# Kernel optimization log

Measured on AMD Instinct MI355X. Metric: run time of the kernel, lower is better.

Reference implementation:

```python
import jax, jax.numpy as jnp
import numpy as np

BN_EPS = 1e-5

def binarize_ste(x):
    # sign() in forward; identity (straight-through) in backward, matching the
    # weight.data / input.data hack in BinarizeConv2d.
    return x + jax.lax.stop_gradient(jnp.sign(x) - x)


def setup_inputs() -> dict:
    key = jax.random.key(0)
    k1, k2, k3, k4 = jax.random.split(key, 4)
    N, Cin, H, W = 16, 32, 224, 224
    Cout, K = 32, 3
    x = jax.random.normal(k1, (N, Cin, H, W), dtype=jnp.float32)
    weight = jax.random.normal(k2, (Cout, Cin, K, K), dtype=jnp.float32) * 0.1
    gamma = jax.random.uniform(k3, (Cout,), dtype=jnp.float32, minval=0.5, maxval=1.5)
    beta = jax.random.normal(k4, (Cout,), dtype=jnp.float32) * 0.1
    return {"x": x, "weight": weight, "gamma": gamma, "beta": beta}


def reference(x, weight, gamma, beta):
    # BinarizeConv2d: binarize input iff C != 3, always binarize weights.
    xb = binarize_ste(x) if x.shape[1] != 3 else x
    wb = binarize_ste(weight)
    y = jax.lax.conv_general_dilated(
        xb, wb,
        window_strides=(1, 1),
        padding=((1, 1), (1, 1)),
        dimension_numbers=("NCHW", "OIHW", "NCHW"),
    )  # [N, Cout, H, W]
    # BatchNorm2d in training mode: per-channel batch statistics over (N, H, W).
    mean = jnp.mean(y, axis=(0, 2, 3))
    var = jnp.var(y, axis=(0, 2, 3))
    inv = jax.lax.rsqrt(var + BN_EPS)
    yn = (y - mean[None, :, None, None]) * inv[None, :, None, None]
    return yn * gamma[None, :, None, None] + beta[None, :, None, None]
```

## Files before the change

### kernel.cpp

```cpp
#include <hip/hip_runtime.h>
#include <stdint.h>

#define NB 16
#define CC 32
#define HH 224
#define WWID 224
#define HWS (HH*WWID)
#define NHWT (NB*HWS)
#define STRIPS (NHWT/4)
#define SPI (HWS/4)
#define SPR (WWID/4)
#define PBLK (STRIPS/256)

#define PITCH 232
#define PROWS 226
#define IMGW (PITCH*PROWS)

typedef float    f4 __attribute__((ext_vector_type(4)));
typedef unsigned u4 __attribute__((ext_vector_type(4)));
typedef unsigned u2 __attribute__((ext_vector_type(2)));

#define WS_WSIGN 0
#define WS_WNZ   2048
#define WS_BASE  4096
#define WS_FLAGW 5248
#define WS_SSUM  5376
#define WS_SSQ   5632
#define WS_BLKF  6144
#define WS_XS    12288
#define WS_XNZ   (12288 + (size_t)NB*IMGW*4)

__global__ void __launch_bounds__(256) pack_x4(
        const float* __restrict__ x, const float* __restrict__ w,
        unsigned* __restrict__ xs, unsigned* __restrict__ xnz,
        unsigned* __restrict__ wsg, unsigned* __restrict__ wnz,
        int* __restrict__ flagw, unsigned* __restrict__ blkflag,
        int* __restrict__ baset, int* __restrict__ s_sum,
        unsigned long long* __restrict__ s_sq) {
    __shared__ unsigned s_sg[288];
    __shared__ int allnz;
    __shared__ unsigned s_zf[4];

    if (blockIdx.x == 0) {
        if (threadIdx.x == 0) allnz = 1;
        if (threadIdx.x < CC) { s_sum[threadIdx.x] = 0; s_sq[threadIdx.x] = 0ull; }
        __syncthreads();
        for (int k = threadIdx.x; k < 288; k += 256) {
            int co = k / 9, tap = k % 9;
            unsigned bits = 0, nz = 0;
            for (int ci = 0; ci < CC; ++ci) {
                float v = w[(co * CC + ci) * 9 + tap];
                bits |= (v > 0.f ? 1u : 0u) << ci;
                nz   |= (v != 0.f ? 1u : 0u) << ci;
            }
            wsg[k] = bits; wnz[k] = nz; s_sg[k] = bits;
            if (nz != 0xffffffffu) atomicAnd(&allnz, 0);
        }
        __syncthreads();
        if (threadIdx.x == 0) *flagw = allnz;
        for (int k = threadIdx.x; k < 288; k += 256) {
            int cls = k >> 5, co = k & 31;
            int hc = cls / 3, wc = cls % 3;
            int nv = 0, corr = 0;
            #pragma unroll
            for (int kh = 0; kh < 3; ++kh)
                #pragma unroll
                for (int kw = 0; kw < 3; ++kw) {
                    bool inv = (hc == 0 && kh == 0) || (hc == 2 && kh == 2) ||
                               (wc == 0 && kw == 0) || (wc == 2 && kw == 2);
                    if (inv) corr += __popc(s_sg[co * 9 + kh * 3 + kw]);
                    else     nv++;
                }
            baset[k] = 32 * nv + 2 * corr;
        }
    }

    int t = blockIdx.x * 256 + threadIdx.x;
    int n = t / SPI, rem = t - n * SPI;
    int h = rem / SPR, w0 = (rem - h * SPR) * 4;
    const float* base = x + (size_t)n * CC * HWS + h * WWID + w0;
    unsigned b0=0,b1=0,b2=0,b3=0, z0=0,z1=0,z2=0,z3=0;
    #pragma unroll
    for (int c = 0; c < CC; ++c) {
        f4 v = __builtin_nontemporal_load((const f4*)(base + (size_t)c * HWS));
        b0 |= (v.x > 0.f ? (1u<<c) : 0u);  z0 |= (v.x != 0.f ? (1u<<c) : 0u);
        b1 |= (v.y > 0.f ? (1u<<c) : 0u);  z1 |= (v.y != 0.f ? (1u<<c) : 0u);
        b2 |= (v.z > 0.f ? (1u<<c) : 0u);  z2 |= (v.z != 0.f ? (1u<<c) : 0u);
        b3 |= (v.w > 0.f ? (1u<<c) : 0u);  z3 |= (v.w != 0.f ? (1u<<c) : 0u);
    }
    size_t rowb = (size_t)n * IMGW + (h + 1) * PITCH;
    size_t d = rowb + 1 + w0;
    xs[d+0]=b0; xs[d+1]=b1; xs[d+2]=b2; xs[d+3]=b3;
    xnz[d+0]=z0; xnz[d+1]=z1; xnz[d+2]=z2; xnz[d+3]=z3;

    if (w0 == 0)        { xs[rowb] = 0;       xnz[rowb] = 0; }
    if (w0 == WWID - 4) { xs[rowb + 225] = 0; xnz[rowb + 225] = 0; }
    if (h == 0) {
        size_t tr = (size_t)n * IMGW;
        #pragma unroll
        for (int j = 0; j < 4; ++j) { xs[tr + 1 + w0 + j] = 0; xnz[tr + 1 + w0 + j] = 0; }
        if (w0 == 0)        { xs[tr] = 0;       xnz[tr] = 0; }
        if (w0 == WWID - 4) { xs[tr + 225] = 0; xnz[tr + 225] = 0; }
    }
    if (h == HH - 1) {
        size_t br = (size_t)n * IMGW + (size_t)(PROWS - 1) * PITCH;
        #pragma unroll
        for (int j = 0; j < 4; ++j) { xs[br + 1 + w0 + j] = 0; xnz[br + 1 + w0 + j] = 0; }
        if (w0 == 0)        { xs[br] = 0;       xnz[br] = 0; }
        if (w0 == WWID - 4) { xs[br + 225] = 0; xnz[br + 225] = 0; }
    }

    bool hasz = (z0 & z1 & z2 & z3) != 0xffffffffu;
    bool anyz = __any(hasz);
    int wid = threadIdx.x >> 6, lane = threadIdx.x & 63;
    if (lane == 0) s_zf[wid] = anyz ? 1u : 0u;
    __syncthreads();
    if (threadIdx.x == 0)
        blkflag[blockIdx.x] = s_zf[0] | s_zf[1] | s_zf[2] | s_zf[3];
}

__device__ __forceinline__ void loadwin(const unsigned* __restrict__ p, unsigned a[6]) {
    u4 lo = *(const u4*)p;
    u2 hi = *(const u2*)(p + 4);
    a[0]=lo.x; a[1]=lo.y; a[2]=lo.z; a[3]=lo.w; a[4]=hi.x; a[5]=hi.y;
}

__device__ __forceinline__ void ad4(const unsigned a0[6], const unsigned a1[6],
                                    const unsigned a2[6],
                                    const unsigned* __restrict__ q, int ad[4]) {
    unsigned q0=q[0],q1=q[1],q2=q[2],q3=q[3],q4=q[4],q5=q[5],q6=q[6],q7=q[7],q8=q[8];
    #pragma unroll
    for (int px = 0; px < 4; ++px) {
        ad[px] = __popc(a0[px]^q0) + __popc(a0[px+1]^q1) + __popc(a0[px+2]^q2)
               + __popc(a1[px]^q3) + __popc(a1[px+1]^q4) + __popc(a1[px+2]^q5)
               + __popc(a2[px]^q6) + __popc(a2[px+1]^q7) + __popc(a2[px+2]^q8);
    }
}

__device__ __forceinline__ void y4_slowc(const unsigned a0[6], const unsigned a1[6],
                                         const unsigned a2[6], const unsigned z0[6],
                                         const unsigned z1[6], const unsigned z2[6],
                                         const unsigned* __restrict__ qs,
                                         const unsigned* __restrict__ qz, int y[4]) {
    #pragma unroll
    for (int px = 0; px < 4; ++px) {
        int am = 0, ad = 0;
        #pragma unroll
        for (int kw = 0; kw < 3; ++kw) {
            unsigned m0 = z0[px+kw] & qz[kw];
            unsigned m1 = z1[px+kw] & qz[3+kw];
            unsigned m2 = z2[px+kw] & qz[6+kw];
            am += __popc(m0) + __popc(m1) + __popc(m2);
            ad += __popc((a0[px+kw]^qs[kw])   & m0)
                + __popc((a1[px+kw]^qs[3+kw]) & m1)
                + __popc((a2[px+kw]^qs[6+kw]) & m2);
        }
        y[px] = am - 2 * ad;
    }
}

__device__ __forceinline__ unsigned zf_load(const unsigned* __restrict__ blkflag, int t) {
    unsigned zv = blkflag[t] | blkflag[t + 256] | blkflag[t + 512];
    if (t < PBLK - 768) zv |= blkflag[t + 768];
    return zv;
}

__device__ __forceinline__ void deswizzle(int B, int* cobase, int* sblk) {
    int xcd = B & 7;
    int r = B >> 3;
    *cobase = (r & 3) * 8;
    *sblk = xcd + 8 * (r >> 2);
}

__global__ void __launch_bounds__(256, 8) convstats(
        const unsigned* __restrict__ xs, const unsigned* __restrict__ xnz,
        const unsigned* __restrict__ wsg, const unsigned* __restrict__ wnz,
        const int* __restrict__ baset, const int* __restrict__ flagw,
        const unsigned* __restrict__ blkflag, int* __restrict__ s_sum,
        unsigned long long* __restrict__ s_sq) {
    __shared__ int sb[288];
    __shared__ unsigned s_zf[4];
    __shared__ int red[4][8][17];

    int cobase, sblk;
    deswizzle(blockIdx.x, &cobase, &sblk);
    int sid = sblk * 256 + threadIdx.x;
    int n = sid / SPI, rem = sid - n * SPI;
    int h = rem / SPR, w0 = (rem - h * SPR) * 4;
    size_t off = (size_t)n * IMGW + h * PITCH + w0;

    unsigned a0[6], a1[6], a2[6];
    loadwin(xs + off, a0); loadwin(xs + off + PITCH, a1); loadwin(xs + off + 2*PITCH, a2);

    int t = threadIdx.x, wid = t >> 6, lane = t & 63;
    unsigned zv = zf_load(blkflag, t);
    int fw = *flagw;
    for (int i = t; i < 288; i += 256) sb[i] = baset[i];
    bool anyz = __any(zv != 0);
    if (lane == 0) s_zf[wid] = anyz ? 1u : 0u;
    __syncthreads();
    bool fast = (fw != 0) && ((s_zf[0] | s_zf[1] | s_zf[2] | s_zf[3]) == 0u);

    int sacc[8], qacc[8];
    if (fast) {
        int hc = (h == 0) ? 0 : ((h == HH-1) ? 6 : 3);
        int c0 = (hc + ((w0 == 0) ? 0 : 1)) * 32;
        int c1 = (hc + 1) * 32;
        int c3 = (hc + ((w0 == WWID-4) ? 2 : 1)) * 32;
        #pragma unroll
        for (int u = 0; u < 8; ++u) {
            int co = cobase + u;
            int ad[4];
            ad4(a0, a1, a2, wsg + co * 9, ad);
            int y0 = sb[c0 + co] - 2 * ad[0];
            int y1 = sb[c1 + co] - 2 * ad[1];
            int y2 = sb[c1 + co] - 2 * ad[2];
            int y3 = sb[c3 + co] - 2 * ad[3];
            sacc[u] = y0 + y1 + y2 + y3;
            qacc[u] = y0*y0 + y1*y1 + y2*y2 + y3*y3;
        }
    } else {
        unsigned z0[6], z1[6], z2[6];
        loadwin(xnz + off, z0); loadwin(xnz + off + PITCH, z1); loadwin(xnz + off + 2*PITCH, z2);
        #pragma unroll
        for (int u = 0; u < 8; ++u) {
            int co = cobase + u;
            int y[4];
            y4_slowc(a0, a1, a2, z0, z1, z2, wsg + co * 9, wnz + co * 9, y);
            sacc[u] = y[0]+y[1]+y[2]+y[3];
            qacc[u] = y[0]*y[0]+y[1]*y[1]+y[2]*y[2]+y[3]*y[3];
        }
    }

    #pragma unroll
    for (int o2 = 32; o2 >= 8; o2 >>= 1) {
        #pragma unroll
        for (int u = 0; u < 8; ++u) {
            sacc[u] += __shfl_down(sacc[u], o2);
            qacc[u] += __shfl_down(qacc[u], o2);
        }
    }
    if (lane < 8) {
        #pragma unroll
        for (int u = 0; u < 8; ++u) {
            red[wid][lane][u]     = sacc[u];
            red[wid][lane][8 + u] = qacc[u];
        }
    }
    __syncthreads();
    if (t < 128) {
        int u16 = t >> 3, s = t & 7;
        int v = red[0][s][u16] + red[1][s][u16] + red[2][s][u16] + red[3][s][u16];
        v += __shfl_down(v, 4); v += __shfl_down(v, 2); v += __shfl_down(v, 1);
        if (s == 0) {
            if (u16 < 8) atomicAdd(&s_sum[cobase + u16], v);
            else         atomicAdd(&s_sq[cobase + u16 - 8],
                                   (unsigned long long)(long long)v);
        }
    }
}

__global__ void __launch_bounds__(256, 8) convnorm(
        const unsigned* __restrict__ xs, const unsigned* __restrict__ xnz,
        const unsigned* __restrict__ wsg, const unsigned* __restrict__ wnz,
        const int* __restrict__ baset, const int* __restrict__ flagw,
        const unsigned* __restrict__ blkflag, const int* __restrict__ s_sum,
        const unsigned long long* __restrict__ s_sq,
        const float* __restrict__ gamma, const float* __restrict__ beta,
        float* __restrict__ out) {
    __shared__ int sb[288];
    __shared__ float s_sc[32], s_sh[32];
    __shared__ unsigned s_zf[4];

    int cobase, sblk;
    deswizzle(blockIdx.x, &cobase, &sblk);
    int sid = sblk * 256 + threadIdx.x;
    int n = sid / SPI, rem = sid - n * SPI;
    int h = rem / SPR, w0 = (rem - h * SPR) * 4;
    size_t off = (size_t)n * IMGW + h * PITCH + w0;

    unsigned a0[6], a1[6], a2[6];
    loadwin(xs + off, a0); loadwin(xs + off + PITCH, a1); loadwin(xs + off + 2*PITCH, a2);

    int t = threadIdx.x, wid = t >> 6, lane = t & 63;
    unsigned zv = zf_load(blkflag, t);
    int fw = *flagw;
    for (int i = t; i < 288; i += 256) sb[i] = baset[i];
    if (t < 32) {
        int c = t;
        double mean = (double)s_sum[c] / (double)NHWT;
        double var  = (double)(long long)s_sq[c] / (double)NHWT - mean * mean;
        float inv = (float)(1.0 / sqrt(var + 1e-5));
        float g = gamma[c] * inv;
        s_sc[c] = g;
        s_sh[c] = beta[c] - (float)mean * g;
    }
    bool anyz = __any(zv != 0);
    if (lane == 0) s_zf[wid] = anyz ? 1u : 0u;
    __syncthreads();
    bool fast = (fw != 0) && ((s_zf[0] | s_zf[1] | s_zf[2] | s_zf[3]) == 0u);

    float* on = out + (size_t)(n * CC + cobase) * HWS + h * WWID + w0;
    if (fast) {
        int hc = (h == 0) ? 0 : ((h == HH-1) ? 6 : 3);
        int c0 = (hc + ((w0 == 0) ? 0 : 1)) * 32;
        int c1 = (hc + 1) * 32;
        int c3 = (hc + ((w0 == WWID-4) ? 2 : 1)) * 32;
        #pragma unroll
        for (int u = 0; u < 8; ++u) {
            int co = cobase + u;
            int ad[4];
            ad4(a0, a1, a2, wsg + co * 9, ad);
            int y0 = sb[c0 + co] - 2 * ad[0];
            int y1 = sb[c1 + co] - 2 * ad[1];
            int y2 = sb[c1 + co] - 2 * ad[2];
            int y3 = sb[c3 + co] - 2 * ad[3];
            float sc = s_sc[co], sh = s_sh[co];
            f4 o = { fmaf((float)y0, sc, sh), fmaf((float)y1, sc, sh),
                     fmaf((float)y2, sc, sh), fmaf((float)y3, sc, sh) };
            *(f4*)(on + (size_t)u * HWS) = o;
        }
    } else {
        unsigned z0[6], z1[6], z2[6];
        loadwin(xnz + off, z0); loadwin(xnz + off + PITCH, z1); loadwin(xnz + off + 2*PITCH, z2);
        #pragma unroll
        for (int u = 0; u < 8; ++u) {
            int co = cobase + u;
            int y[4];
            y4_slowc(a0, a1, a2, z0, z1, z2, wsg + co * 9, wnz + co * 9, y);
            float sc = s_sc[co], sh = s_sh[co];
            f4 o = { fmaf((float)y[0], sc, sh), fmaf((float)y[1], sc, sh),
                     fmaf((float)y[2], sc, sh), fmaf((float)y[3], sc, sh) };
            *(f4*)(on + (size_t)u * HWS) = o;
        }
    }
}

extern "C" void kernel_launch(void* const* d_in, const int* in_sizes, int n_in,
                              void* d_out, int out_size, void* d_ws, size_t ws_size,
                              hipStream_t stream) {
    const float* x     = (const float*)d_in[0];
    const float* w     = (const float*)d_in[1];
    const float* gamma = (const float*)d_in[2];
    const float* beta  = (const float*)d_in[3];
    float* out = (float*)d_out;

    char* ws = (char*)d_ws;
    unsigned* wsg            = (unsigned*)(ws + WS_WSIGN);
    unsigned* wnz            = (unsigned*)(ws + WS_WNZ);
    int* baset               = (int*)(ws + WS_BASE);
    int* flagw               = (int*)(ws + WS_FLAGW);
    int* s_sum               = (int*)(ws + WS_SSUM);
    unsigned long long* s_sq = (unsigned long long*)(ws + WS_SSQ);
    unsigned* blkflag        = (unsigned*)(ws + WS_BLKF);
    unsigned* xsb            = (unsigned*)(ws + WS_XS);
    unsigned* xzb            = (unsigned*)(ws + WS_XNZ);

    int cgrid = PBLK * 4;
    pack_x4  <<<PBLK, 256, 0, stream>>>(x, w, xsb, xzb, wsg, wnz,
                                        flagw, blkflag, baset, s_sum, s_sq);
    convstats<<<cgrid, 256, 0, stream>>>(xsb, xzb, wsg, wnz, baset, flagw, blkflag,
                                         s_sum, s_sq);
    convnorm <<<cgrid, 256, 0, stream>>>(xsb, xzb, wsg, wnz, baset, flagw, blkflag,
                                         s_sum, s_sq, gamma, beta, out);
}
```

Before: 77.97 us.

## Process two strip blocks per thread block in conv kernels, halving grid

Both convstats and convnorm now loop over two strip blocks per thread block, and the launch grid is halved. This amortizes per-block setup (flag OR-reduction, LDS table fill, barrier, BN coefficient computation), and in the stats kernel it halves the reduction and atomic traffic. The trade-off is fewer resident waves per CU, which reduces latency hiding for loads and the large output stores.

Result: slower. 83.98 us (+7.7%).

```diff
diff --git a/kernel.cpp b/kernel.cpp
--- a/kernel.cpp
+++ b/kernel.cpp
@@ -165,11 +165,11 @@
     return zv;
 }
 
-__device__ __forceinline__ void deswizzle(int B, int* cobase, int* sblk) {
+__device__ __forceinline__ void deswizzle2(int B, int* cobase, int* sblk0) {
     int xcd = B & 7;
     int r = B >> 3;
     *cobase = (r & 3) * 8;
-    *sblk = xcd + 8 * (r >> 2);
+    *sblk0 = xcd + 8 * (r >> 2);
 }
 
 __global__ void __launch_bounds__(256, 8) convstats(
@@ -182,15 +182,8 @@
     __shared__ unsigned s_zf[4];
     __shared__ int red[4][8][17];
 
-    int cobase, sblk;
-    deswizzle(blockIdx.x, &cobase, &sblk);
-    int sid = sblk * 256 + threadIdx.x;
-    int n = sid / SPI, rem = sid - n * SPI;
-    int h = rem / SPR, w0 = (rem - h * SPR) * 4;
-    size_t off = (size_t)n * IMGW + h * PITCH + w0;
-
-    unsigned a0[6], a1[6], a2[6];
-    loadwin(xs + off, a0); loadwin(xs + off + PITCH, a1); loadwin(xs + off + 2*PITCH, a2);
+    int cobase, sblk0;
+    deswizzle2(blockIdx.x, &cobase, &sblk0);
 
     int t = threadIdx.x, wid = t >> 6, lane = t & 63;
     unsigned zv = zf_load(blkflag, t);
@@ -202,33 +195,48 @@
     bool fast = (fw != 0) && ((s_zf[0] | s_zf[1] | s_zf[2] | s_zf[3]) == 0u);
 
     int sacc[8], qacc[8];
-    if (fast) {
-        int hc = (h == 0) ? 0 : ((h == HH-1) ? 6 : 3);
-        int c0 = (hc + ((w0 == 0) ? 0 : 1)) * 32;
-        int c1 = (hc + 1) * 32;
-        int c3 = (hc + ((w0 == WWID-4) ? 2 : 1)) * 32;
-        #pragma unroll
-        for (int u = 0; u < 8; ++u) {
-            int co = cobase + u;
-            int ad[4];
-            ad4(a0, a1, a2, wsg + co * 9, ad);
-            int y0 = sb[c0 + co] - 2 * ad[0];
-            int y1 = sb[c1 + co] - 2 * ad[1];
-            int y2 = sb[c1 + co] - 2 * ad[2];
-            int y3 = sb[c3 + co] - 2 * ad[3];
-            sacc[u] = y0 + y1 + y2 + y3;
-            qacc[u] = y0*y0 + y1*y1 + y2*y2 + y3*y3;
-        }
-    } else {
-        unsigned z0[6], z1[6], z2[6];
-        loadwin(xnz + off, z0); loadwin(xnz + off + PITCH, z1); loadwin(xnz + off + 2*PITCH, z2);
-        #pragma unroll
-        for (int u = 0; u < 8; ++u) {
-            int co = cobase + u;
-            int y[4];
-            y4_slowc(a0, a1, a2, z0, z1, z2, wsg + co * 9, wnz + co * 9, y);
-            sacc[u] = y[0]+y[1]+y[2]+y[3];
-            qacc[u] = y[0]*y[0]+y[1]*y[1]+y[2]*y[2]+y[3]*y[3];
+    #pragma unroll
+    for (int u = 0; u < 8; ++u) { sacc[u] = 0; qacc[u] = 0; }
+
+    #pragma unroll 1
+    for (int it = 0; it < 2; ++it) {
+        int sblk = sblk0 + it * 392;
+        int sid = sblk * 256 + t;
+        int n = sid / SPI, rem = sid - n * SPI;
+        int h = rem / SPR, w0 = (rem - h * SPR) * 4;
+        size_t off = (size_t)n * IMGW + h * PITCH + w0;
+
+        unsigned a0[6], a1[6], a2[6];
+        loadwin(xs + off, a0); loadwin(xs + off + PITCH, a1); loadwin(xs + off + 2*PITCH, a2);
+
+        if (fast) {
+            int hc = (h == 0) ? 0 : ((h == HH-1) ? 6 : 3);
+            int c0 = (hc + ((w0 == 0) ? 0 : 1)) * 32;
+            int c1 = (hc + 1) * 32;
+            int c3 = (hc + ((w0 == WWID-4) ? 2 : 1)) * 32;
+            #pragma unroll
+            for (int u = 0; u < 8; ++u) {
+                int co = cobase + u;
+                int ad[4];
+                ad4(a0, a1, a2, wsg + co * 9, ad);
+                int y0 = sb[c0 + co] - 2 * ad[0];
+                int y1 = sb[c1 + co] - 2 * ad[1];
+                int y2 = sb[c1 + co] - 2 * ad[2];
+                int y3 = sb[c3 + co] - 2 * ad[3];
+                sacc[u] += y0 + y1 + y2 + y3;
+                qacc[u] += y0*y0 + y1*y1 + y2*y2 + y3*y3;
+            }
+        } else {
+            unsigned z0[6], z1[6], z2[6];
+            loadwin(xnz + off, z0); loadwin(xnz + off + PITCH, z1); loadwin(xnz + off + 2*PITCH, z2);
+            #pragma unroll
+            for (int u = 0; u < 8; ++u) {
+                int co = cobase + u;
+                int y[4];
+                y4_slowc(a0, a1, a2, z0, z1, z2, wsg + co * 9, wnz + co * 9, y);
+                sacc[u] += y[0]+y[1]+y[2]+y[3];
+                qacc[u] += y[0]*y[0]+y[1]*y[1]+y[2]*y[2]+y[3]*y[3];
+            }
         }
     }
 
@@ -272,15 +280,8 @@
     __shared__ float s_sc[32], s_sh[32];
     __shared__ unsigned s_zf[4];
 
-    int cobase, sblk;
-    deswizzle(blockIdx.x, &cobase, &sblk);
-    int sid = sblk * 256 + threadIdx.x;
-    int n = sid / SPI, rem = sid - n * SPI;
-    int h = rem / SPR, w0 = (rem - h * SPR) * 4;
-    size_t off = (size_t)n * IMGW + h * PITCH + w0;
-
-    unsigned a0[6], a1[6], a2[6];
-    loadwin(xs + off, a0); loadwin(xs + off + PITCH, a1); loadwin(xs + off + 2*PITCH, a2);
+    int cobase, sblk0;
+    deswizzle2(blockIdx.x, &cobase, &sblk0);
 
     int t = threadIdx.x, wid = t >> 6, lane = t & 63;
     unsigned zv = zf_load(blkflag, t);
@@ -300,38 +301,50 @@
     __syncthreads();
     bool fast = (fw != 0) && ((s_zf[0] | s_zf[1] | s_zf[2] | s_zf[3]) == 0u);
 
-    float* on = out + (size_t)(n * CC + cobase) * HWS + h * WWID + w0;
-    if (fast) {
-        int hc = (h == 0) ? 0 : ((h == HH-1) ? 6 : 3);
-        int c0 = (hc + ((w0 == 0) ? 0 : 1)) * 32;
-        int c1 = (hc + 1) * 32;
-        int c3 = (hc + ((w0 == WWID-4) ? 2 : 1)) * 32;
-        #pragma unroll
-        for (int u = 0; u < 8; ++u) {
-            int co = cobase + u;
-            int ad[4];
-            ad4(a0, a1, a2, wsg + co * 9, ad);
-            int y0 = sb[c0 + co] - 2 * ad[0];
-            int y1 = sb[c1 + co] - 2 * ad[1];
-            int y2 = sb[c1 + co] - 2 * ad[2];
-            int y3 = sb[c3 + co] - 2 * ad[3];
-            float sc = s_sc[co], sh = s_sh[co];
-            f4 o = { fmaf((float)y0, sc, sh), fmaf((float)y1, sc, sh),
-                     fmaf((float)y2, sc, sh), fmaf((float)y3, sc, sh) };
-            *(f4*)(on + (size_t)u * HWS) = o;
-        }
-    } else {
-        unsigned z0[6], z1[6], z2[6];
-        loadwin(xnz + off, z0); loadwin(xnz + off + PITCH, z1); loadwin(xnz + off + 2*PITCH, z2);
-        #pragma unroll
-        for (int u = 0; u < 8; ++u) {
-            int co = cobase + u;
-            int y[4];
-            y4_slowc(a0, a1, a2, z0, z1, z2, wsg + co * 9, wnz + co * 9, y);
-            float sc = s_sc[co], sh = s_sh[co];
-            f4 o = { fmaf((float)y[0], sc, sh), fmaf((float)y[1], sc, sh),
-                     fmaf((float)y[2], sc, sh), fmaf((float)y[3], sc, sh) };
-            *(f4*)(on + (size_t)u * HWS) = o;
+    #pragma unroll 1
+    for (int it = 0; it < 2; ++it) {
+        int sblk = sblk0 + it * 392;
+        int sid = sblk * 256 + t;
+        int n = sid / SPI, rem = sid - n * SPI;
+        int h = rem / SPR, w0 = (rem - h * SPR) * 4;
+        size_t off = (size_t)n * IMGW + h * PITCH + w0;
+
+        unsigned a0[6], a1[6], a2[6];
+        loadwin(xs + off, a0); loadwin(xs + off + PITCH, a1); loadwin(xs + off + 2*PITCH, a2);
+
+        float* on = out + (size_t)(n * CC + cobase) * HWS + h * WWID + w0;
+        if (fast) {
+            int hc = (h == 0) ? 0 : ((h == HH-1) ? 6 : 3);
+            int c0 = (hc + ((w0 == 0) ? 0 : 1)) * 32;
+            int c1 = (hc + 1) * 32;
+            int c3 = (hc + ((w0 == WWID-4) ? 2 : 1)) * 32;
+            #pragma unroll
+            for (int u = 0; u < 8; ++u) {
+                int co = cobase + u;
+                int ad[4];
+                ad4(a0, a1, a2, wsg + co * 9, ad);
+                int y0 = sb[c0 + co] - 2 * ad[0];
+                int y1 = sb[c1 + co] - 2 * ad[1];
+                int y2 = sb[c1 + co] - 2 * ad[2];
+                int y3 = sb[c3 + co] - 2 * ad[3];
+                float sc = s_sc[co], sh = s_sh[co];
+                f4 o = { fmaf((float)y0, sc, sh), fmaf((float)y1, sc, sh),
+                         fmaf((float)y2, sc, sh), fmaf((float)y3, sc, sh) };
+                *(f4*)(on + (size_t)u * HWS) = o;
+            }
+        } else {
+            unsigned z0[6], z1[6], z2[6];
+            loadwin(xnz + off, z0); loadwin(xnz + off + PITCH, z1); loadwin(xnz + off + 2*PITCH, z2);
+            #pragma unroll
+            for (int u = 0; u < 8; ++u) {
+                int co = cobase + u;
+                int y[4];
+                y4_slowc(a0, a1, a2, z0, z1, z2, wsg + co * 9, wnz + co * 9, y);
+                float sc = s_sc[co], sh = s_sh[co];
+                f4 o = { fmaf((float)y[0], sc, sh), fmaf((float)y[1], sc, sh),
+                         fmaf((float)y[2], sc, sh), fmaf((float)y[3], sc, sh) };
+                *(f4*)(on + (size_t)u * HWS) = o;
+            }
         }
     }
 }
@@ -356,7 +369,7 @@
     unsigned* xsb            = (unsigned*)(ws + WS_XS);
     unsigned* xzb            = (unsigned*)(ws + WS_XNZ);
 
-    int cgrid = PBLK * 4;
+    int cgrid = PBLK * 2;
     pack_x4  <<<PBLK, 256, 0, stream>>>(x, w, xsb, xzb, wsg, wnz,
                                         flagw, blkflag, baset, s_sum, s_sq);
     convstats<<<cgrid, 256, 0, stream>>>(xsb, xzb, wsg, wnz, baset, flagw, blkflag,
```
